# Performance work log

Hardware: AMD Instinct MI355X
Metric: run time of the kernel (lower is better)

## Reference

```python
import jax, jax.numpy as jnp
import numpy as np

N_NODES = 50000
N_EDGES = 800000
IN_CH = 128
HID = 128


def setup_inputs() -> dict:
    key = jax.random.key(0)
    ks = jax.random.split(key, 8)
    s = 0.05
    x = jax.random.normal(ks[0], (N_NODES, IN_CH), dtype=jnp.float32)
    edge_index = jax.random.randint(ks[1], (2, N_EDGES), 0, N_NODES, dtype=jnp.int64)
    W1l = jax.random.normal(ks[2], (IN_CH, HID), dtype=jnp.float32) * s
    W1r = jax.random.normal(ks[3], (IN_CH, HID), dtype=jnp.float32) * s
    b1 = jnp.zeros((HID,), dtype=jnp.float32)
    W2l = jax.random.normal(ks[4], (HID, HID), dtype=jnp.float32) * s
    W2r = jax.random.normal(ks[5], (HID, HID), dtype=jnp.float32) * s
    b2 = jnp.zeros((HID,), dtype=jnp.float32)
    Wout = jax.random.normal(ks[6], (HID, 2), dtype=jnp.float32) * s
    bout = jnp.zeros((2,), dtype=jnp.float32)
    return {"x": x, "edge_index": edge_index, "W1l": W1l, "W1r": W1r, "b1": b1,
            "W2l": W2l, "W2r": W2r, "b2": b2, "Wout": Wout, "bout": bout}


def _mean_aggr(h, src, dst, n_nodes):
    # mean of neighbor (source) features per destination node (PyG SAGEConv default)
    msg_sum = jax.ops.segment_sum(h[src], dst, num_segments=n_nodes)  # [N, D]
    deg = jax.ops.segment_sum(jnp.ones((src.shape[0],), dtype=h.dtype), dst,
                              num_segments=n_nodes)  # [N]
    return msg_sum / jnp.maximum(deg, 1.0)[:, None]


def _sage_conv(h, src, dst, Wl, Wr, b, n_nodes):
    aggr = _mean_aggr(h, src, dst, n_nodes)
    return aggr @ Wl + h @ Wr + b


def reference(x, edge_index, W1l, W1r, b1, W2l, W2r, b2, Wout, bout):
    n = x.shape[0]
    src, dst = edge_index[0], edge_index[1]
    h = jax.nn.relu(_sage_conv(x, src, dst, W1l, W1r, b1, n))
    # dropout is identity in inference mode
    h = jax.nn.relu(_sage_conv(h, src, dst, W2l, W2r, b2, n))
    logits = h @ Wout + bout
    return (logits, h)
```

## Files before the change

### kernel.cpp

```cpp
#include <hip/hip_runtime.h>

#define NN 50000
#define NE 800000
#define CH 128
#define CAP 64
#define NCHUNK ((NE + 255) / 256)
#define EDGE_BLK (NCHUNK * 8)

typedef __attribute__((ext_vector_type(8))) short short8;
typedef __attribute__((ext_vector_type(4))) float float4a;

#define DEG_OFF  0
#define CSR_OFF  50048
#define XB_OFF   1650048
#define AGB_OFF  4850048
#define H1B_OFF  8050048
#define WTP_OFF  11250048

static __device__ __forceinline__ unsigned short f2b(float f) {
    unsigned u = __float_as_uint(f);
    unsigned r = u + 0x7fff + ((u >> 16) & 1);
    return (unsigned short)(r >> 16);
}

__global__ __launch_bounds__(256) void k_build(
    const int* __restrict__ eidx, int* __restrict__ deg,
    unsigned short* __restrict__ csr,
    const float* __restrict__ W1l, const float* __restrict__ W1r,
    const float* __restrict__ W2l, const float* __restrict__ W2r,
    unsigned short* __restrict__ wtp,
    const float* __restrict__ x, unsigned* __restrict__ xb) {
    int b = blockIdx.x;
    if (b < EDGE_BLK) {
        int p = b & 7;
        int e = (b >> 3) * 256 + threadIdx.x;
        if (e < NE) {
            int src = eidx[e];
            int dst = eidx[NE + e];
            if ((unsigned)src < NN && (unsigned)dst < NN && (dst & 7) == p) {
                int r = atomicAdd(&deg[dst], 1);
                r = min(r, CAP - 1);
                csr[(size_t)dst * CAP + r] = (unsigned short)src;
            }
        }
    } else {
        int i = (b - EDGE_BLK) * 256 + threadIdx.x;
        if (i < 65536) {
            int layer = i >> 15;
            int li = i & 32767;
            int e = li & 7, lane = (li >> 3) & 63, j = (li >> 9) & 7, kt = li >> 12;
            int ln = lane & 15, quad = lane >> 4;
            int n = j * 16 + ln;
            int k = kt * 32 + quad * 8 + e;
            const float* Wl = layer ? W2l : W1l;
            const float* Wr = layer ? W2r : W1r;
            float v = (k < 128) ? Wl[k * 128 + n] : Wr[(k - 128) * 128 + n];
            wtp[(size_t)layer * 32768 + li] = f2b(v);
        } else {
            int i2 = i - 65536;
            if (i2 < NN * (CH / 2)) {
                float2 v = ((const float2*)x)[i2];
                xb[i2] = (unsigned)f2b(v.x) | ((unsigned)f2b(v.y) << 16);
            }
        }
    }
}

static __device__ __forceinline__ void acc8(float* acc, uint4 v) {
    acc[0] += __uint_as_float(v.x << 16); acc[1] += __uint_as_float(v.x & 0xffff0000u);
    acc[2] += __uint_as_float(v.y << 16); acc[3] += __uint_as_float(v.y & 0xffff0000u);
    acc[4] += __uint_as_float(v.z << 16); acc[5] += __uint_as_float(v.z & 0xffff0000u);
    acc[6] += __uint_as_float(v.w << 16); acc[7] += __uint_as_float(v.w & 0xffff0000u);
}

__global__ __launch_bounds__(256) void k_gather4(
    const int* __restrict__ deg, const unsigned short* __restrict__ csr,
    const uint4* __restrict__ featb, uint4* __restrict__ aggrb) {
    int wave = (blockIdx.x * 256 + threadIdx.x) >> 6;
    int lane = threadIdx.x & 63;
    if (wave >= NN) return;
    int d = min(deg[wave], CAP);
    const unsigned short* row = csr + (size_t)wave * CAP;
    int g = lane >> 4;
    int c = lane & 15;

    float acc[8];
    #pragma unroll
    for (int e = 0; e < 8; ++e) acc[e] = 0.0f;

    int i0 = 0;
    for (; i0 + 16 <= d; i0 += 16) {
        int s1 = row[i0 + g];
        int s2 = row[i0 + 4 + g];
        int s3 = row[i0 + 8 + g];
        int s4 = row[i0 + 12 + g];
        uint4 v1 = featb[(size_t)s1 * 16 + c];
        uint4 v2 = featb[(size_t)s2 * 16 + c];
        uint4 v3 = featb[(size_t)s3 * 16 + c];
        uint4 v4 = featb[(size_t)s4 * 16 + c];
        acc8(acc, v1); acc8(acc, v2); acc8(acc, v3); acc8(acc, v4);
    }
    for (; i0 + 8 <= d; i0 += 8) {
        int s1 = row[i0 + g];
        int s2 = row[i0 + 4 + g];
        uint4 v1 = featb[(size_t)s1 * 16 + c];
        uint4 v2 = featb[(size_t)s2 * 16 + c];
        acc8(acc, v1); acc8(acc, v2);
    }
    if (i0 < d) {
        int n1 = i0 + g, n2 = i0 + 4 + g;
        int s1 = (n1 < d) ? (int)row[n1] : 0;
        int s2 = (n2 < d) ? (int)row[n2] : 0;
        uint4 v1 = featb[(size_t)s1 * 16 + c];
        uint4 v2 = featb[(size_t)s2 * 16 + c];
        if (n1 < d) acc8(acc, v1);
        if (n2 < d) acc8(acc, v2);
    }

    #pragma unroll
    for (int e = 0; e < 8; ++e) {
        acc[e] += __shfl_xor(acc[e], 32, 64);
        acc[e] += __shfl_xor(acc[e], 16, 64);
    }
    if (lane < 16) {
        float s = 1.0f / (float)(d > 1 ? d : 1);
        uint4 o;
        o.x = (unsigned)f2b(acc[0] * s) | ((unsigned)f2b(acc[1] * s) << 16);
        o.y = (unsigned)f2b(acc[2] * s) | ((unsigned)f2b(acc[3] * s) << 16);
        o.z = (unsigned)f2b(acc[4] * s) | ((unsigned)f2b(acc[5] * s) << 16);
        o.w = (unsigned)f2b(acc[6] * s) | ((unsigned)f2b(acc[7] * s) << 16);
        aggrb[(size_t)wave * 16 + c] = o;
    }
}

template <bool BF16OUT>
__global__ __launch_bounds__(256) void k_layer_mfma(
    const short* __restrict__ aggrb, const short* __restrict__ hinb,
    const short* __restrict__ wtp, const float* __restrict__ bias,
    float* __restrict__ outf, unsigned short* __restrict__ outb,
    const float* __restrict__ Wout, const float* __restrict__ bout,
    float* __restrict__ logits) {
    int lane = threadIdx.x & 63;
    int wid = threadIdx.x >> 6;
    int m0 = blockIdx.x * 64 + wid * 16;
    int ln = lane & 15;
    int quad = lane >> 4;
    int m = m0 + ln;
    int mc = min(m, NN - 1);

    float4a acc[8];
    #pragma unroll
    for (int j = 0; j < 8; ++j) acc[j] = (float4a){0.0f, 0.0f, 0.0f, 0.0f};

    #pragma unroll
    for (int kt = 0; kt < 8; ++kt) {
        const short* arow = (kt < 4 ? aggrb : hinb) + (size_t)mc * CH + (kt & 3) * 32 + quad * 8;
        short8 av = *(const short8*)arow;
        const short* bk = wtp + (size_t)kt * 4096 + lane * 8;
        #pragma unroll
        for (int j = 0; j < 8; ++j) {
            short8 bv = *(const short8*)(bk + j * 512);
            acc[j] = __builtin_amdgcn_mfma_f32_16x16x32_bf16(av, bv, acc[j], 0, 0, 0);
        }
    }

    float p0[4], p1[4];
    #pragma unroll
    for (int r = 0; r < 4; ++r) { p0[r] = 0.0f; p1[r] = 0.0f; }

    #pragma unroll
    for (int j = 0; j < 8; ++j) {
        int col = j * 16 + ln;
        float bj = bias[col];
        float w0 = 0.0f, w1 = 0.0f;
        if (!BF16OUT) { w0 = Wout[col * 2]; w1 = Wout[col * 2 + 1]; }
        #pragma unroll
        for (int r = 0; r < 4; ++r) {
            int row = m0 + quad * 4 + r;
            float v = fmaxf(acc[j][r] + bj, 0.0f);
            if (row < NN) {
                if (BF16OUT) outb[(size_t)row * CH + col] = f2b(v);
                else         outf[(size_t)row * CH + col] = v;
            }
            if (!BF16OUT) { p0[r] = fmaf(v, w0, p0[r]); p1[r] = fmaf(v, w1, p1[r]); }
        }
    }

    if (!BF16OUT) {
        #pragma unroll
        for (int r = 0; r < 4; ++r) {
            #pragma unroll
            for (int off = 1; off < 16; off <<= 1) {
                p0[r] += __shfl_xor(p0[r], off, 64);
                p1[r] += __shfl_xor(p1[r], off, 64);
            }
        }
        if (ln == 0) {
            float b0 = bout[0], b1 = bout[1];
            #pragma unroll
            for (int r = 0; r < 4; ++r) {
                int row = m0 + quad * 4 + r;
                if (row < NN) {
                    logits[row * 2 + 0] = p0[r] + b0;
                    logits[row * 2 + 1] = p1[r] + b1;
                }
            }
        }
    }
}

extern "C" void kernel_launch(void* const* d_in, const int* in_sizes, int n_in,
                              void* d_out, int out_size, void* d_ws, size_t ws_size,
                              hipStream_t stream) {
    const float* x    = (const float*)d_in[0];
    const int*   eidx = (const int*)d_in[1];
    const float* W1l  = (const float*)d_in[2];
    const float* W1r  = (const float*)d_in[3];
    const float* b1   = (const float*)d_in[4];
    const float* W2l  = (const float*)d_in[5];
    const float* W2r  = (const float*)d_in[6];
    const float* b2   = (const float*)d_in[7];
    const float* Wout = (const float*)d_in[8];
    const float* bout = (const float*)d_in[9];

    float* out    = (float*)d_out;
    float* ws     = (float*)d_ws;
    int*   deg    = (int*)ws;
    unsigned short* csr = (unsigned short*)(ws + CSR_OFF);
    unsigned* xb  = (unsigned*)(ws + XB_OFF);
    unsigned* agb = (unsigned*)(ws + AGB_OFF);
    unsigned* h1b = (unsigned*)(ws + H1B_OFF);
    unsigned short* wtp = (unsigned short*)(ws + WTP_OFF);
    float* logits = out;
    float* hout   = out + 100000;

    hipMemsetAsync(deg, 0, NN * sizeof(int), stream);

    int prep_blocks = (65536 + NN * (CH / 2) + 255) / 256;
    k_build<<<EDGE_BLK + prep_blocks, 256, 0, stream>>>(eidx, deg, csr,
                                                        W1l, W1r, W2l, W2r, wtp, x, xb);

    k_gather4<<<(NN + 3) / 4, 256, 0, stream>>>(deg, csr, (const uint4*)xb, (uint4*)agb);
    k_layer_mfma<true><<<(NN + 63) / 64, 256, 0, stream>>>(
        (const short*)agb, (const short*)xb, (const short*)wtp, b1,
        nullptr, (unsigned short*)h1b, nullptr, nullptr, nullptr);

    k_gather4<<<(NN + 3) / 4, 256, 0, stream>>>(deg, csr, (const uint4*)h1b, (uint4*)agb);
    k_layer_mfma<false><<<(NN + 63) / 64, 256, 0, stream>>>(
        (const short*)agb, (const short*)h1b, (const short*)(wtp + 32768), b2,
        hout, nullptr, Wout, bout, logits);
}
```

Baseline: 233.0 us.

## Fuse neighbor gather into MFMA layer kernel via shared memory staging

Merges the mean-aggregation gather and the MFMA linear layer into one kernel per layer. Each wave aggregates its 16 nodes into LDS, which then feeds the MFMA A operand, so the aggregated bf16 intermediate no longer makes a round trip through global memory. Also moves the prep blocks ahead of the edge blocks in the build kernel and uses nontemporal loads and stores for the x conversion and the final fp32 output. The risk is lower gather parallelism: the grid drops from about 12.5k to about 780 blocks, and each wave processes 16 nodes serially, which may hide memory latency less well.

After: 271.7 us. 1.17x slower.

```diff
diff --git a/kernel.cpp b/kernel.cpp
--- a/kernel.cpp
+++ b/kernel.cpp
@@ -6,6 +6,8 @@
 #define CAP 64
 #define NCHUNK ((NE + 255) / 256)
 #define EDGE_BLK (NCHUNK * 8)
+#define PREP_ITEMS (65536 + NN * (CH / 2))
+#define PREP_BLK ((((PREP_ITEMS + 255) / 256) + 7) & ~7)
 
 typedef __attribute__((ext_vector_type(8))) short short8;
 typedef __attribute__((ext_vector_type(4))) float float4a;
@@ -13,9 +15,8 @@
 #define DEG_OFF  0
 #define CSR_OFF  50048
 #define XB_OFF   1650048
-#define AGB_OFF  4850048
-#define H1B_OFF  8050048
-#define WTP_OFF  11250048
+#define H1B_OFF  4850048
+#define WTP_OFF  8050048
 
 static __device__ __forceinline__ unsigned short f2b(float f) {
     unsigned u = __float_as_uint(f);
@@ -31,9 +32,10 @@
     unsigned short* __restrict__ wtp,
     const float* __restrict__ x, unsigned* __restrict__ xb) {
     int b = blockIdx.x;
-    if (b < EDGE_BLK) {
-        int p = b & 7;
-        int e = (b >> 3) * 256 + threadIdx.x;
+    if (b >= PREP_BLK) {
+        int eb = b - PREP_BLK;
+        int p = eb & 7;
+        int e = (eb >> 3) * 256 + threadIdx.x;
         if (e < NE) {
             int src = eidx[e];
             int dst = eidx[NE + e];
@@ -44,7 +46,7 @@
             }
         }
     } else {
-        int i = (b - EDGE_BLK) * 256 + threadIdx.x;
+        int i = b * 256 + threadIdx.x;
         if (i < 65536) {
             int layer = i >> 15;
             int li = i & 32767;
@@ -56,12 +58,14 @@
             const float* Wr = layer ? W2r : W1r;
             float v = (k < 128) ? Wl[k * 128 + n] : Wr[(k - 128) * 128 + n];
             wtp[(size_t)layer * 32768 + li] = f2b(v);
-        } else {
+        } else if (i < PREP_ITEMS) {
             int i2 = i - 65536;
-            if (i2 < NN * (CH / 2)) {
-                float2 v = ((const float2*)x)[i2];
-                xb[i2] = (unsigned)f2b(v.x) | ((unsigned)f2b(v.y) << 16);
-            }
+            unsigned long long pr =
+                __builtin_nontemporal_load((const unsigned long long*)x + i2);
+            float lo = __uint_as_float((unsigned)pr);
+            float hi = __uint_as_float((unsigned)(pr >> 32));
+            unsigned pk = (unsigned)f2b(lo) | ((unsigned)f2b(hi) << 16);
+            __builtin_nontemporal_store(pk, &xb[i2]);
         }
     }
 }
@@ -73,80 +77,79 @@
     acc[6] += __uint_as_float(v.w << 16); acc[7] += __uint_as_float(v.w & 0xffff0000u);
 }
 
-__global__ __launch_bounds__(256) void k_gather4(
+template <bool BF16OUT>
+__global__ __launch_bounds__(256) void k_gl(
     const int* __restrict__ deg, const unsigned short* __restrict__ csr,
-    const uint4* __restrict__ featb, uint4* __restrict__ aggrb) {
-    int wave = (blockIdx.x * 256 + threadIdx.x) >> 6;
-    int lane = threadIdx.x & 63;
-    if (wave >= NN) return;
-    int d = min(deg[wave], CAP);
-    const unsigned short* row = csr + (size_t)wave * CAP;
-    int g = lane >> 4;
-    int c = lane & 15;
-
-    float acc[8];
-    #pragma unroll
-    for (int e = 0; e < 8; ++e) acc[e] = 0.0f;
-
-    int i0 = 0;
-    for (; i0 + 16 <= d; i0 += 16) {
-        int s1 = row[i0 + g];
-        int s2 = row[i0 + 4 + g];
-        int s3 = row[i0 + 8 + g];
-        int s4 = row[i0 + 12 + g];
-        uint4 v1 = featb[(size_t)s1 * 16 + c];
-        uint4 v2 = featb[(size_t)s2 * 16 + c];
-        uint4 v3 = featb[(size_t)s3 * 16 + c];
-        uint4 v4 = featb[(size_t)s4 * 16 + c];
-        acc8(acc, v1); acc8(acc, v2); acc8(acc, v3); acc8(acc, v4);
-    }
-    for (; i0 + 8 <= d; i0 += 8) {
-        int s1 = row[i0 + g];
-        int s2 = row[i0 + 4 + g];
-        uint4 v1 = featb[(size_t)s1 * 16 + c];
-        uint4 v2 = featb[(size_t)s2 * 16 + c];
-        acc8(acc, v1); acc8(acc, v2);
-    }
-    if (i0 < d) {
-        int n1 = i0 + g, n2 = i0 + 4 + g;
-        int s1 = (n1 < d) ? (int)row[n1] : 0;
-        int s2 = (n2 < d) ? (int)row[n2] : 0;
-        uint4 v1 = featb[(size_t)s1 * 16 + c];
-        uint4 v2 = featb[(size_t)s2 * 16 + c];
-        if (n1 < d) acc8(acc, v1);
-        if (n2 < d) acc8(acc, v2);
-    }
-
-    #pragma unroll
-    for (int e = 0; e < 8; ++e) {
-        acc[e] += __shfl_xor(acc[e], 32, 64);
-        acc[e] += __shfl_xor(acc[e], 16, 64);
-    }
-    if (lane < 16) {
-        float s = 1.0f / (float)(d > 1 ? d : 1);
-        uint4 o;
-        o.x = (unsigned)f2b(acc[0] * s) | ((unsigned)f2b(acc[1] * s) << 16);
-        o.y = (unsigned)f2b(acc[2] * s) | ((unsigned)f2b(acc[3] * s) << 16);
-        o.z = (unsigned)f2b(acc[4] * s) | ((unsigned)f2b(acc[5] * s) << 16);
-        o.w = (unsigned)f2b(acc[6] * s) | ((unsigned)f2b(acc[7] * s) << 16);
-        aggrb[(size_t)wave * 16 + c] = o;
-    }
-}
-
-template <bool BF16OUT>
-__global__ __launch_bounds__(256) void k_layer_mfma(
-    const short* __restrict__ aggrb, const short* __restrict__ hinb,
+    const uint4* __restrict__ featb, const short* __restrict__ hinb,
     const short* __restrict__ wtp, const float* __restrict__ bias,
     float* __restrict__ outf, unsigned short* __restrict__ outb,
     const float* __restrict__ Wout, const float* __restrict__ bout,
     float* __restrict__ logits) {
+    __shared__ uint4 aS[64][17];
     int lane = threadIdx.x & 63;
-    int wid = threadIdx.x >> 6;
-    int m0 = blockIdx.x * 64 + wid * 16;
+    int w = threadIdx.x >> 6;
+    int node0 = blockIdx.x * 64 + w * 16;
+    int g = lane >> 4;
+    int c = lane & 15;
+
+    for (int m = 0; m < 16; ++m) {
+        int node = node0 + m;
+        int d = (node < NN) ? min(deg[node], CAP) : 0;
+        const unsigned short* row = csr + (size_t)node * CAP;
+
+        float acc[8];
+        #pragma unroll
+        for (int e = 0; e < 8; ++e) acc[e] = 0.0f;
+
+        int i0 = 0;
+        for (; i0 + 16 <= d; i0 += 16) {
+            int s1 = row[i0 + g];
+            int s2 = row[i0 + 4 + g];
+            int s3 = row[i0 + 8 + g];
+            int s4 = row[i0 + 12 + g];
+            uint4 v1 = featb[(size_t)s1 * 16 + c];
+            uint4 v2 = featb[(size_t)s2 * 16 + c];
+            uint4 v3 = featb[(size_t)s3 * 16 + c];
+            uint4 v4 = featb[(size_t)s4 * 16 + c];
+            acc8(acc, v1); acc8(acc, v2); acc8(acc, v3); acc8(acc, v4);
+        }
+        for (; i0 + 8 <= d; i0 += 8) {
+            int s1 = row[i0 + g];
+            int s2 = row[i0 + 4 + g];
+            uint4 v1 = featb[(size_t)s1 * 16 + c];
+            uint4 v2 = featb[(size_t)s2 * 16 + c];
+            acc8(acc, v1); acc8(acc, v2);
+        }
+        if (i0 < d) {
+            int n1 = i0 + g, n2 = i0 + 4 + g;
+            int s1 = (n1 < d) ? (int)row[n1] : 0;
+            int s2 = (n2 < d) ? (int)row[n2] : 0;
+            uint4 v1 = featb[(size_t)s1 * 16 + c];
+            uint4 v2 = featb[(size_t)s2 * 16 + c];
+            if (n1 < d) acc8(acc, v1);
+            if (n2 < d) acc8(acc, v2);
+        }
+
+        #pragma unroll
+        for (int e = 0; e < 8; ++e) {
+            acc[e] += __shfl_xor(acc[e], 32, 64);
+            acc[e] += __shfl_xor(acc[e], 16, 64);
+        }
+        if (lane < 16) {
+            float s = 1.0f / (float)(d > 1 ? d : 1);
+            uint4 o;
+            o.x = (unsigned)f2b(acc[0] * s) | ((unsigned)f2b(acc[1] * s) << 16);
+            o.y = (unsigned)f2b(acc[2] * s) | ((unsigned)f2b(acc[3] * s) << 16);
+            o.z = (unsigned)f2b(acc[4] * s) | ((unsigned)f2b(acc[5] * s) << 16);
+            o.w = (unsigned)f2b(acc[6] * s) | ((unsigned)f2b(acc[7] * s) << 16);
+            aS[w * 16 + m][c] = o;
+        }
+    }
+    __syncthreads();
+
     int ln = lane & 15;
     int quad = lane >> 4;
-    int m = m0 + ln;
-    int mc = min(m, NN - 1);
+    int mc = min(node0 + ln, NN - 1);
 
     float4a acc[8];
     #pragma unroll
@@ -154,8 +157,9 @@
 
     #pragma unroll
     for (int kt = 0; kt < 8; ++kt) {
-        const short* arow = (kt < 4 ? aggrb : hinb) + (size_t)mc * CH + (kt & 3) * 32 + quad * 8;
-        short8 av = *(const short8*)arow;
+        short8 av;
+        if (kt < 4) av = *(const short8*)&aS[w * 16 + ln][(kt << 2) + quad];
+        else av = *(const short8*)(hinb + (size_t)mc * CH + (kt & 3) * 32 + quad * 8);
         const short* bk = wtp + (size_t)kt * 4096 + lane * 8;
         #pragma unroll
         for (int j = 0; j < 8; ++j) {
@@ -176,11 +180,11 @@
         if (!BF16OUT) { w0 = Wout[col * 2]; w1 = Wout[col * 2 + 1]; }
         #pragma unroll
         for (int r = 0; r < 4; ++r) {
-            int row = m0 + quad * 4 + r;
+            int row = node0 + quad * 4 + r;
             float v = fmaxf(acc[j][r] + bj, 0.0f);
             if (row < NN) {
                 if (BF16OUT) outb[(size_t)row * CH + col] = f2b(v);
-                else         outf[(size_t)row * CH + col] = v;
+                else         __builtin_nontemporal_store(v, &outf[(size_t)row * CH + col]);
             }
             if (!BF16OUT) { p0[r] = fmaf(v, w0, p0[r]); p1[r] = fmaf(v, w1, p1[r]); }
         }
@@ -199,7 +203,7 @@
             float b0 = bout[0], b1 = bout[1];
             #pragma unroll
             for (int r = 0; r < 4; ++r) {
-                int row = m0 + quad * 4 + r;
+                int row = node0 + quad * 4 + r;
                 if (row < NN) {
                     logits[row * 2 + 0] = p0[r] + b0;
                     logits[row * 2 + 1] = p1[r] + b1;
@@ -228,25 +232,22 @@
     int*   deg    = (int*)ws;
     unsigned short* csr = (unsigned short*)(ws + CSR_OFF);
     unsigned* xb  = (unsigned*)(ws + XB_OFF);
-    unsigned* agb = (unsigned*)(ws + AGB_OFF);
     unsigned* h1b = (unsigned*)(ws + H1B_OFF);
     unsigned short* wtp = (unsigned short*)(ws + WTP_OFF);
     float* logits = out;
     float* hout   = out + 100000;
 
-    hipMemsetAsync(deg, 0, NN * sizeof(int), stream);
-
-    int prep_blocks = (65536 + NN * (CH / 2) + 255) / 256;
-    k_build<<<EDGE_BLK + prep_blocks, 256, 0, stream>>>(eidx, deg, csr,
-                                                        W1l, W1r, W2l, W2r, wtp, x, xb);
-
-    k_gather4<<<(NN + 3) / 4, 256, 0, stream>>>(deg, csr, (const uint4*)xb, (uint4*)agb);
-    k_layer_mfma<true><<<(NN + 63) / 64, 256, 0, stream>>>(
-        (const short*)agb, (const short*)xb, (const short*)wtp, b1,
+    (void)hipMemsetAsync(deg, 0, NN * sizeof(int), stream);
+
+    k_build<<<PREP_BLK + EDGE_BLK, 256, 0, stream>>>(eidx, deg, csr,
+                                                     W1l, W1r, W2l, W2r, wtp, x, xb);
+
+    k_gl<true><<<(NN + 63) / 64, 256, 0, stream>>>(
+        deg, csr, (const uint4*)xb, (const short*)xb, (const short*)wtp, b1,
         nullptr, (unsigned short*)h1b, nullptr, nullptr, nullptr);
 
-    k_gather4<<<(NN + 3) / 4, 256, 0, stream>>>(deg, csr, (const uint4*)h1b, (uint4*)agb);
-    k_layer_mfma<false><<<(NN + 63) / 64, 256, 0, stream>>>(
-        (const short*)agb, (const short*)h1b, (const short*)(wtp + 32768), b2,
+    k_gl<false><<<(NN + 63) / 64, 256, 0, stream>>>(
+        deg, csr, (const uint4*)h1b, (const short*)h1b,
+        (const short*)(wtp + 32768), b2,
         hout, nullptr, Wout, bout, logits);
 }
```
